# Kernel tuning notes

Hardware: AMD Instinct MI355X
Metric: run time of the kernel (lower is better)

Reference implementation:

```python
import jax, jax.numpy as jnp
import numpy as np

N_TEST = 16384
NUM_CLASSES = 1000
TEMPERATURE = 2.0


def setup_inputs() -> dict:
    key = jax.random.key(0)
    ks = jax.random.split(key, 6)
    mk = lambda k: jax.random.normal(k, (N_TEST, NUM_CLASSES), dtype=jnp.float32)
    return {
        "outputs1": mk(ks[0]),
        "outputs2": mk(ks[1]),
        "outputs3": mk(ks[2]),
        "outputs4": mk(ks[3]),
        "mimic": mk(ks[4]),
        "targets": jax.random.randint(ks[5], (N_TEST,), 0, NUM_CLASSES, dtype=jnp.int64),
        "n_test": N_TEST,
    }


def _margin(o, targets):
    # top-2 reduction replaces the full descending sort (same top-2 values)
    top2, _ = jax.lax.top_k(o, 2)                                   # [n, 2]
    tgt_val = jnp.take_along_axis(o, targets[:, None], axis=1)[:, 0]  # [n]
    # margin = (max - second_max) only when target is the argmax value, else 0
    return jnp.where(top2[:, 0] == tgt_val, top2[:, 0] - top2[:, 1], jnp.zeros((), o.dtype))


def reference(outputs1, outputs2, outputs3, outputs4, mimic, targets, n_test):
    outs = (outputs1, outputs2, outputs3, outputs4, mimic)
    preds = jnp.stack([_margin(o, targets) for o in outs], axis=1)  # [n, 5]
    out_threshold = jax.nn.softmax(preds / TEMPERATURE, axis=1)
    max_preds = jnp.max(jnp.stack((outputs1, outputs2, outputs3, outputs4), axis=0))
    return max_preds, out_threshold
```

## Files before the change

### kernel.cpp

```cpp
#include <hip/hip_runtime.h>
#include <math.h>

#define NCLS 1000
#define NV4  250
#define INV_TEMP 0.5f

__global__ __launch_bounds__(256) void margins_kernel(
    const float* __restrict__ o1, const float* __restrict__ o2,
    const float* __restrict__ o3, const float* __restrict__ o4,
    const float* __restrict__ mim, const int* __restrict__ targets,
    float* __restrict__ out, float* __restrict__ blockmax, int n)
{
    const int lane = threadIdx.x & 63;
    const int wid  = threadIdx.x >> 6;
    const int row  = blockIdx.x * 4 + wid;
    __shared__ float smax[4];

    float gm = -INFINITY;
    const float* mats[5] = {o1, o2, o3, o4, mim};

    float preds[5];

    if (row < n) {
        const int tgt = targets[row];
        #pragma unroll
        for (int m = 0; m < 5; ++m) {
            const float*  rowp = mats[m] + (size_t)row * NCLS;
            const float4* p4   = (const float4*)rowp;
            float m1 = -INFINITY, m2 = -INFINITY;
            #pragma unroll
            for (int it = 0; it < 4; ++it) {
                const int idx = lane + it * 64;
                if (idx < NV4) {
                    float4 v = p4[idx];
                    m2 = fmaxf(m2, fminf(m1, v.x)); m1 = fmaxf(m1, v.x);
                    m2 = fmaxf(m2, fminf(m1, v.y)); m1 = fmaxf(m1, v.y);
                    m2 = fmaxf(m2, fminf(m1, v.z)); m1 = fmaxf(m1, v.z);
                    m2 = fmaxf(m2, fminf(m1, v.w)); m1 = fmaxf(m1, v.w);
                    if (m < 4) {
                        gm = fmaxf(gm, fmaxf(fmaxf(v.x, v.y), fmaxf(v.z, v.w)));
                    }
                }
            }
            #pragma unroll
            for (int off = 32; off > 0; off >>= 1) {
                float q1 = __shfl_xor(m1, off, 64);
                float q2 = __shfl_xor(m2, off, 64);
                m2 = fmaxf(fmaxf(m2, q2), fminf(m1, q1));
                m1 = fmaxf(m1, q1);
            }
            const float tv = rowp[tgt];
            preds[m] = (m1 == tv) ? (m1 - m2) : 0.0f;
        }

        const float p0 = preds[0] * INV_TEMP, p1 = preds[1] * INV_TEMP,
                    p2 = preds[2] * INV_TEMP, p3 = preds[3] * INV_TEMP,
                    p4 = preds[4] * INV_TEMP;
        const float pm = fmaxf(fmaxf(fmaxf(p0, p1), fmaxf(p2, p3)), p4);
        const float e0 = expf(p0 - pm), e1 = expf(p1 - pm), e2 = expf(p2 - pm),
                    e3 = expf(p3 - pm), e4 = expf(p4 - pm);
        const float inv = 1.0f / (e0 + e1 + e2 + e3 + e4);
        if (lane == 0) {
            float* b = out + 1 + (size_t)row * 5;
            b[0] = e0 * inv; b[1] = e1 * inv; b[2] = e2 * inv;
            b[3] = e3 * inv; b[4] = e4 * inv;
        }
    }

    #pragma unroll
    for (int off = 32; off > 0; off >>= 1)
        gm = fmaxf(gm, __shfl_xor(gm, off, 64));
    if (lane == 0) smax[wid] = gm;
    __syncthreads();
    if (threadIdx.x == 0) {
        blockmax[blockIdx.x] =
            fmaxf(fmaxf(smax[0], smax[1]), fmaxf(smax[2], smax[3]));
    }
}

__global__ __launch_bounds__(256) void final_max_kernel(
    const float* __restrict__ blockmax, int nblocks, float* __restrict__ out)
{
    float m = -INFINITY;
    for (int i = threadIdx.x; i < nblocks; i += 256) m = fmaxf(m, blockmax[i]);
    #pragma unroll
    for (int off = 32; off > 0; off >>= 1)
        m = fmaxf(m, __shfl_xor(m, off, 64));
    __shared__ float s[4];
    const int lane = threadIdx.x & 63, wid = threadIdx.x >> 6;
    if (lane == 0) s[wid] = m;
    __syncthreads();
    if (threadIdx.x == 0)
        out[0] = fmaxf(fmaxf(s[0], s[1]), fmaxf(s[2], s[3]));
}

extern "C" void kernel_launch(void* const* d_in, const int* in_sizes, int n_in,
                              void* d_out, int out_size, void* d_ws, size_t ws_size,
                              hipStream_t stream) {
    const float* o1  = (const float*)d_in[0];
    const float* o2  = (const float*)d_in[1];
    const float* o3  = (const float*)d_in[2];
    const float* o4  = (const float*)d_in[3];
    const float* mim = (const float*)d_in[4];
    const int*   tgt = (const int*)d_in[5];
    const int n = in_sizes[5];

    float* out = (float*)d_out;
    float* ws  = (float*)d_ws;

    const int blocks = (n + 3) / 4;
    margins_kernel<<<blocks, 256, 0, stream>>>(o1, o2, o3, o4, mim, tgt, out, ws, n);
    final_max_kernel<<<1, 256, 0, stream>>>(ws, blocks, out);
}
```

Before: 298.0 us.

## Split work to one wavefront per row-matrix pair with separate softmax pass

Each wavefront now handles a single (row, matrix) pair instead of all five matrices for one row. This gives five times more wavefronts, all four loads issued up front, and a tree-style top-2 merge. Margins go to workspace, and a new softmax kernel computes the per-row softmax and also does a two-stage reduction of the block maxima. The aim is more memory-level parallelism and occupancy for a bandwidth-bound pass. The cost is an extra kernel launch and a small workspace round trip, and the row count is now hardcoded at compile time.

```diff
diff --git a/kernel.cpp b/kernel.cpp
--- a/kernel.cpp
+++ b/kernel.cpp
@@ -1,97 +1,117 @@
 #include <hip/hip_runtime.h>
 #include <math.h>
 
-#define NCLS 1000
-#define NV4  250
+#define NCLS  1000
+#define NV4   250
+#define NROWS 16384
 #define INV_TEMP 0.5f
+#define NEG_INF (-INFINITY)
+
+__device__ __forceinline__ void merge2(float& a1, float& a2, float b1, float b2) {
+    const float mn = fminf(a1, b1);
+    a1 = fmaxf(a1, b1);
+    a2 = fmaxf(mn, fmaxf(a2, b2));
+}
 
 __global__ __launch_bounds__(256) void margins_kernel(
     const float* __restrict__ o1, const float* __restrict__ o2,
     const float* __restrict__ o3, const float* __restrict__ o4,
     const float* __restrict__ mim, const int* __restrict__ targets,
-    float* __restrict__ out, float* __restrict__ blockmax, int n)
+    float* __restrict__ ws_margin, float* __restrict__ blockmax)
 {
     const int lane = threadIdx.x & 63;
     const int wid  = threadIdx.x >> 6;
-    const int row  = blockIdx.x * 4 + wid;
+    const int pair = blockIdx.x * 4 + wid;
+    const int row  = pair / 5;
+    const int mat  = pair - row * 5;
     __shared__ float smax[4];
 
-    float gm = -INFINITY;
-    const float* mats[5] = {o1, o2, o3, o4, mim};
+    const float* base = (mat == 0) ? o1 : (mat == 1) ? o2 : (mat == 2) ? o3
+                      : (mat == 3) ? o4 : mim;
+    const float*  rowp = base + (size_t)row * NCLS;
+    const float4* p4   = (const float4*)rowp;
 
-    float preds[5];
+    const int tgt = targets[row];
+    const float tv = rowp[tgt];
+    float4 v0 = p4[lane];
+    float4 v1 = p4[64  + lane];
+    float4 v2 = p4[128 + lane];
+    float4 v3 = p4[(lane < 58) ? (192 + lane) : 249];
+    if (lane >= 58) v3 = make_float4(NEG_INF, NEG_INF, NEG_INF, NEG_INF);
 
-    if (row < n) {
-        const int tgt = targets[row];
-        #pragma unroll
-        for (int m = 0; m < 5; ++m) {
-            const float*  rowp = mats[m] + (size_t)row * NCLS;
-            const float4* p4   = (const float4*)rowp;
-            float m1 = -INFINITY, m2 = -INFINITY;
-            #pragma unroll
-            for (int it = 0; it < 4; ++it) {
-                const int idx = lane + it * 64;
-                if (idx < NV4) {
-                    float4 v = p4[idx];
-                    m2 = fmaxf(m2, fminf(m1, v.x)); m1 = fmaxf(m1, v.x);
-                    m2 = fmaxf(m2, fminf(m1, v.y)); m1 = fmaxf(m1, v.y);
-                    m2 = fmaxf(m2, fminf(m1, v.z)); m1 = fmaxf(m1, v.z);
-                    m2 = fmaxf(m2, fminf(m1, v.w)); m1 = fmaxf(m1, v.w);
-                    if (m < 4) {
-                        gm = fmaxf(gm, fmaxf(fmaxf(v.x, v.y), fmaxf(v.z, v.w)));
-                    }
-                }
-            }
-            #pragma unroll
-            for (int off = 32; off > 0; off >>= 1) {
-                float q1 = __shfl_xor(m1, off, 64);
-                float q2 = __shfl_xor(m2, off, 64);
-                m2 = fmaxf(fmaxf(m2, q2), fminf(m1, q1));
-                m1 = fmaxf(m1, q1);
-            }
-            const float tv = rowp[tgt];
-            preds[m] = (m1 == tv) ? (m1 - m2) : 0.0f;
-        }
+    float t1[4], t2[4];
+    const float4 vv[4] = {v0, v1, v2, v3};
+    #pragma unroll
+    for (int i = 0; i < 4; ++i) {
+        const float hi1 = fmaxf(vv[i].x, vv[i].y), lo1 = fminf(vv[i].x, vv[i].y);
+        const float hi2 = fmaxf(vv[i].z, vv[i].w), lo2 = fminf(vv[i].z, vv[i].w);
+        t1[i] = fmaxf(hi1, hi2);
+        t2[i] = fmaxf(fminf(hi1, hi2), fmaxf(lo1, lo2));
+    }
+    merge2(t1[0], t2[0], t1[1], t2[1]);
+    merge2(t1[2], t2[2], t1[3], t2[3]);
+    merge2(t1[0], t2[0], t1[2], t2[2]);
+    float m1 = t1[0], m2 = t2[0];
 
-        const float p0 = preds[0] * INV_TEMP, p1 = preds[1] * INV_TEMP,
-                    p2 = preds[2] * INV_TEMP, p3 = preds[3] * INV_TEMP,
-                    p4 = preds[4] * INV_TEMP;
+    #pragma unroll
+    for (int off = 32; off >= 1; off >>= 1) {
+        const float q1 = __shfl_xor(m1, off, 64);
+        const float q2 = __shfl_xor(m2, off, 64);
+        merge2(m1, m2, q1, q2);
+    }
+
+    if (lane == 0) {
+        ws_margin[pair] = (m1 == tv) ? (m1 - m2) : 0.0f;
+        smax[wid] = (mat < 4) ? m1 : NEG_INF;
+    }
+    __syncthreads();
+    if (threadIdx.x == 0)
+        blockmax[blockIdx.x] =
+            fmaxf(fmaxf(smax[0], smax[1]), fmaxf(smax[2], smax[3]));
+}
+
+__global__ __launch_bounds__(256) void softmax_kernel(
+    const float* __restrict__ ws_margin, const float* __restrict__ blockmax,
+    float* __restrict__ out, float* __restrict__ stage2, int nblocks)
+{
+    const int row = blockIdx.x * 256 + threadIdx.x;
+    if (row < NROWS) {
+        const float* pr = ws_margin + (size_t)row * 5;
+        const float p0 = pr[0] * INV_TEMP, p1 = pr[1] * INV_TEMP,
+                    p2 = pr[2] * INV_TEMP, p3 = pr[3] * INV_TEMP,
+                    p4 = pr[4] * INV_TEMP;
         const float pm = fmaxf(fmaxf(fmaxf(p0, p1), fmaxf(p2, p3)), p4);
         const float e0 = expf(p0 - pm), e1 = expf(p1 - pm), e2 = expf(p2 - pm),
                     e3 = expf(p3 - pm), e4 = expf(p4 - pm);
         const float inv = 1.0f / (e0 + e1 + e2 + e3 + e4);
-        if (lane == 0) {
-            float* b = out + 1 + (size_t)row * 5;
-            b[0] = e0 * inv; b[1] = e1 * inv; b[2] = e2 * inv;
-            b[3] = e3 * inv; b[4] = e4 * inv;
-        }
+        float* b = out + 1 + (size_t)row * 5;
+        b[0] = e0 * inv; b[1] = e1 * inv; b[2] = e2 * inv;
+        b[3] = e3 * inv; b[4] = e4 * inv;
     }
 
+    float m = NEG_INF;
+    for (int i = blockIdx.x * 320 + threadIdx.x, e = min((int)((blockIdx.x + 1) * 320), nblocks);
+         i < e; i += 256)
+        m = fmaxf(m, blockmax[i]);
     #pragma unroll
-    for (int off = 32; off > 0; off >>= 1)
-        gm = fmaxf(gm, __shfl_xor(gm, off, 64));
-    if (lane == 0) smax[wid] = gm;
-    __syncthreads();
-    if (threadIdx.x == 0) {
-        blockmax[blockIdx.x] =
-            fmaxf(fmaxf(smax[0], smax[1]), fmaxf(smax[2], smax[3]));
-    }
-}
-
-__global__ __launch_bounds__(256) void final_max_kernel(
-    const float* __restrict__ blockmax, int nblocks, float* __restrict__ out)
-{
-    float m = -INFINITY;
-    for (int i = threadIdx.x; i < nblocks; i += 256) m = fmaxf(m, blockmax[i]);
-    #pragma unroll
-    for (int off = 32; off > 0; off >>= 1)
+    for (int off = 32; off >= 1; off >>= 1)
         m = fmaxf(m, __shfl_xor(m, off, 64));
     __shared__ float s[4];
     const int lane = threadIdx.x & 63, wid = threadIdx.x >> 6;
     if (lane == 0) s[wid] = m;
     __syncthreads();
     if (threadIdx.x == 0)
-        out[0] = fmaxf(fmaxf(s[0], s[1]), fmaxf(s[2], s[3]));
+        stage2[blockIdx.x] = fmaxf(fmaxf(s[0], s[1]), fmaxf(s[2], s[3]));
+}
+
+__global__ __launch_bounds__(64) void final_max_kernel(
+    const float* __restrict__ stage2, int n, float* __restrict__ out)
+{
+    float m = (threadIdx.x < n) ? stage2[threadIdx.x] : NEG_INF;
+    #pragma unroll
+    for (int off = 32; off >= 1; off >>= 1)
+        m = fmaxf(m, __shfl_xor(m, off, 64));
+    if (threadIdx.x == 0) out[0] = m;
 }
 
 extern "C" void kernel_launch(void* const* d_in, const int* in_sizes, int n_in,
@@ -103,12 +123,15 @@
     const float* o4  = (const float*)d_in[3];
     const float* mim = (const float*)d_in[4];
     const int*   tgt = (const int*)d_in[5];
-    const int n = in_sizes[5];
 
     float* out = (float*)d_out;
-    float* ws  = (float*)d_ws;
+    float* ws_margin = (float*)d_ws;
+    const int nblocks = (NROWS * 5) / 4;
+    float* blockmax = ws_margin + NROWS * 5;
+    float* stage2   = blockmax + nblocks;
 
-    const int blocks = (n + 3) / 4;
-    margins_kernel<<<blocks, 256, 0, stream>>>(o1, o2, o3, o4, mim, tgt, out, ws, n);
-    final_max_kernel<<<1, 256, 0, stream>>>(ws, blocks, out);
+    margins_kernel<<<nblocks, 256, 0, stream>>>(o1, o2, o3, o4, mim, tgt,
+                                                ws_margin, blockmax);
+    softmax_kernel<<<64, 256, 0, stream>>>(ws_margin, blockmax, out, stage2, nblocks);
+    final_max_kernel<<<1, 64, 0, stream>>>(stage2, 64, out);
 }
```

After: 293.5 us. No clear change (-1.5%).
